# Kernel optimization log

Hardware: AMD Instinct MI355X
Metric: run time of the kernel (lower is better)

Reference implementation:

```python
import jax, jax.numpy as jnp
import numpy as np

B, N, D = 4, 1024, 1024
H, DK, DV = 8, 128, 128
EPS = 1e-6


def setup_inputs() -> dict:
    key = jax.random.key(0)
    ks = jax.random.split(key, 16)
    s = 0.02
    return {
        "q_time": jax.random.normal(ks[0], (B, N, D), jnp.float32),
        "k_time": jax.random.normal(ks[1], (B, N, D), jnp.float32),
        "q_feature": jax.random.normal(ks[2], (B, N, D), jnp.float32),
        "k_feature": jax.random.normal(ks[3], (B, N, D), jnp.float32),
        "v": jax.random.normal(ks[4], (B, N, D), jnp.float32),
        "attn_mask": jax.random.randint(ks[5], (B, N, N), 0, 2, jnp.int32),
        "w_qs_time": jax.random.normal(ks[6], (H * DK, D), jnp.float32) * s,
        "w_ks_time": jax.random.normal(ks[7], (H * DK, D), jnp.float32) * s,
        "w_qs_feature": jax.random.normal(ks[8], (H * DV, D), jnp.float32) * s,
        "w_ks_feature": jax.random.normal(ks[9], (H * DV, D), jnp.float32) * s,
        "w_vs": jax.random.normal(ks[10], (H * DV, D), jnp.float32) * s,
        "w_fc": jax.random.normal(ks[11], (D, H * DV), jnp.float32) * s,
        "ln_gamma": jnp.ones((D,), jnp.float32),
        "ln_beta": jnp.zeros((D,), jnp.float32),
    }


def reference(q_time, k_time, q_feature, k_feature, v, attn_mask,
              w_qs_time, w_ks_time, w_qs_feature, w_ks_feature, w_vs,
              w_fc, ln_gamma, ln_beta):
    temp = DK ** 0.5
    residual = v

    def proj(x, w, d):
        # [B,N,D] @ [D, H*d] -> [B,H,N,d]
        return (x @ w.T).reshape(B, N, H, d).transpose(0, 2, 1, 3)

    qt = proj(q_time, w_qs_time, DK)
    kt = proj(k_time, w_ks_time, DK)
    qf = proj(q_feature, w_qs_feature, DV)
    kf = proj(k_feature, w_ks_feature, DV)
    vv = proj(v, w_vs, DV)

    # time attention: [B,H,N,N]
    attn_time = jnp.einsum('bhnd,bhmd->bhnm', qt / temp, kt)
    attn_time = jnp.where(attn_mask[:, None, :, :] == 0, -1e9, attn_time)
    attn_time = jax.nn.softmax(attn_time, axis=-1)

    # feature attention: q_feature^T @ k_feature -> [B,H,DV,DV]
    attn_feature = jnp.einsum('bhnd,bhne->bhde', qf / temp, kf)
    attn_feature = jax.nn.softmax(attn_feature, axis=-1)

    # chained matmuls: (attn_time @ v) @ attn_feature -> [B,H,N,DV]
    out = jnp.einsum('bhnm,bhmd->bhnd', attn_time, vv)
    out = jnp.einsum('bhnd,bhde->bhne', out, attn_feature)

    out = out.transpose(0, 2, 1, 3).reshape(B, N, H * DV)
    out = out @ w_fc.T + residual  # dropout = identity (eval)

    mean = jnp.mean(out, axis=-1, keepdims=True)
    var = jnp.var(out, axis=-1, keepdims=True)
    out = (out - mean) / jnp.sqrt(var + EPS) * ln_gamma + ln_beta
    return out, attn_time, attn_feature
```

## Files before the change

kernel.cpp:

```cpp
#include <hip/hip_runtime.h>
#include <hip/hip_bf16.h>
#include <cstdint>
#include <cstddef>

typedef unsigned short u16;
typedef unsigned int u32;
typedef short v8s __attribute__((ext_vector_type(8)));
typedef float v4f __attribute__((ext_vector_type(4)));
typedef __hip_bfloat16 bf16;

#define PROJ_ELEMS  4194304ull
#define AT_ELEMS    33554432ull
#define INV_TEMP    0.08838834764831845f

#define GLOBAL_AS __attribute__((address_space(1)))
#define LDS_AS    __attribute__((address_space(3)))

__device__ __forceinline__ void store_out(float* p, float v) { *p = v; }
__device__ __forceinline__ void store_out(bf16* p, float v) { *p = __float2bfloat16(v); }

__device__ __forceinline__ v8s load8f(const float* p) {
    const float4 a = *(const float4*)p;
    const float4 b = *(const float4*)(p + 4);
    v8s r;
    bf16 t;
    t = __float2bfloat16(a.x); r[0] = *(const short*)&t;
    t = __float2bfloat16(a.y); r[1] = *(const short*)&t;
    t = __float2bfloat16(a.z); r[2] = *(const short*)&t;
    t = __float2bfloat16(a.w); r[3] = *(const short*)&t;
    t = __float2bfloat16(b.x); r[4] = *(const short*)&t;
    t = __float2bfloat16(b.y); r[5] = *(const short*)&t;
    t = __float2bfloat16(b.z); r[6] = *(const short*)&t;
    t = __float2bfloat16(b.w); r[7] = *(const short*)&t;
    return r;
}

template <typename AT, typename OutT>
__device__ __forceinline__ void gemm_core(
    const AT* __restrict__ Ab, const u16* __restrict__ Bb, OutT* __restrict__ Cb,
    int K, int lda, int ldb, int ldc, float alpha, int m0, int n0)
{
    __shared__ __align__(16) u16 sA[128][32];
    __shared__ __align__(16) u16 sB[128][32];

    const int tid  = threadIdx.x;
    const int lane = tid & 63;
    const int wid  = tid >> 6;
    const int wm = (wid >> 1) * 64;
    const int wn = (wid & 1) * 64;
    const int quad = lane >> 4;
    const int l16  = lane & 15;

    v4f acc[4][4];
    #pragma unroll
    for (int i = 0; i < 4; ++i)
        #pragma unroll
        for (int j = 0; j < 4; ++j)
            acc[i][j] = (v4f){0.f, 0.f, 0.f, 0.f};

    for (int k0 = 0; k0 < K; k0 += 32) {
        #pragma unroll
        for (int it = 0; it < 2; ++it) {
            const int slot = tid + it * 256;
            const int row  = slot >> 2;
            const int cg   = (slot & 3) << 3;
            __builtin_amdgcn_global_load_lds(
                (const GLOBAL_AS void*)(Bb + (size_t)(n0 + row) * (size_t)ldb + (size_t)(k0 + cg)),
                (LDS_AS void*)((char*)&sB[0][0] + slot * 16), 16, 0, 0);
            if constexpr (sizeof(AT) == 2) {
                __builtin_amdgcn_global_load_lds(
                    (const GLOBAL_AS void*)((const u16*)Ab + (size_t)(m0 + row) * (size_t)lda + (size_t)(k0 + cg)),
                    (LDS_AS void*)((char*)&sA[0][0] + slot * 16), 16, 0, 0);
            } else {
                *(v8s*)&sA[row][cg] =
                    load8f((const float*)Ab + (size_t)(m0 + row) * (size_t)lda + (size_t)(k0 + cg));
            }
        }
        __syncthreads();

        v8s af[4], bfr[4];
        #pragma unroll
        for (int i = 0; i < 4; ++i) {
            af[i]  = *(const v8s*)&sA[wm + i * 16 + l16][quad * 8];
            bfr[i] = *(const v8s*)&sB[wn + i * 16 + l16][quad * 8];
        }
        #pragma unroll
        for (int i = 0; i < 4; ++i)
            #pragma unroll
            for (int j = 0; j < 4; ++j)
                acc[i][j] = __builtin_amdgcn_mfma_f32_16x16x32_bf16(af[i], bfr[j], acc[i][j], 0, 0, 0);
        __syncthreads();
    }

    #pragma unroll
    for (int i = 0; i < 4; ++i) {
        int rbase = m0 + wm + i * 16 + quad * 4;
        #pragma unroll
        for (int j = 0; j < 4; ++j) {
            int gcol = n0 + wn + j * 16 + l16;
            #pragma unroll
            for (int r = 0; r < 4; ++r)
                store_out(&Cb[(size_t)(rbase + r) * (size_t)ldc + (size_t)gcol],
                          acc[i][j][r] * alpha);
        }
    }
}

template <typename AT, typename OutT>
__global__ __launch_bounds__(256, 2)
void gemm_fast(const AT* __restrict__ A, const u16* __restrict__ B, OutT* __restrict__ C,
               int K, int lda, int ldb, int ldc, int batDiv,
               long long sAo, long long sAi, long long sBo, long long sBi,
               long long sCo, long long sCi, float alpha)
{
    const int z  = blockIdx.z;
    const int zo = z / batDiv;
    const int zi = z - zo * batDiv;
    gemm_core<AT, OutT>(A + (size_t)zo * (size_t)sAo + (size_t)zi * (size_t)sAi,
                        B + (size_t)zo * (size_t)sBo + (size_t)zi * (size_t)sBi,
                        C + (size_t)zo * (size_t)sCo + (size_t)zi * (size_t)sCi,
                        K, lda, ldb, ldc, alpha, blockIdx.y * 128, blockIdx.x * 128);
}

struct P5 { const u16* a[5]; };
__global__ __launch_bounds__(256, 2)
void gemm_proj5(P5 As, const u16* __restrict__ W, u16* __restrict__ C)
{
    const int z = blockIdx.z;
    gemm_core<u16, bf16>(As.a[z], W + (size_t)z * 1048576ull,
                         (bf16*)(C + (size_t)z * PROJ_ELEMS),
                         1024, 1024, 1024, 1024, 1.f, blockIdx.y * 128, blockIdx.x * 128);
}

__global__ __launch_bounds__(256, 2)
void gemm_feat_sk(const u16* __restrict__ qfT, const u16* __restrict__ kfT, float* __restrict__ Fp)
{
    const int kc = blockIdx.x, z = blockIdx.y;
    gemm_core<u16, float>(qfT + (size_t)z * 131072ull + (size_t)kc * 128ull,
                          kfT + (size_t)z * 131072ull + (size_t)kc * 128ull,
                          Fp + ((size_t)kc * 32 + z) * 16384ull,
                          128, 1024, 1024, 128, INV_TEMP, 0, 0);
}

template <int NT> struct CP { const float* p[NT]; };

template <int NT>
__global__ __launch_bounds__(256)
void cvt_batch(CP<NT> ps, u16* __restrict__ dst, int perElems)
{
    const float* s = ps.p[blockIdx.z];
    u16* d = dst + (size_t)blockIdx.z * (size_t)perElems;
    const int i = (blockIdx.x * 256 + threadIdx.x) * 8;
    *(v8s*)(d + i) = load8f(s + i);
}

__global__ __launch_bounds__(256)
void mask_pack(const int* __restrict__ mask, u32* __restrict__ mb)
{
    const int w = blockIdx.x * 256 + threadIdx.x;
    const int* src = mask + (size_t)w * 32ull;
    u32 bits = 0;
    #pragma unroll
    for (int i = 0; i < 32; i += 4) {
        int4 v = *(const int4*)(src + i);
        bits |= (u32)(v.x != 0) << i;
        bits |= (u32)(v.y != 0) << (i + 1);
        bits |= (u32)(v.z != 0) << (i + 2);
        bits |= (u32)(v.w != 0) << (i + 3);
    }
    mb[w] = bits;
}

struct T3 { const u16* in[3]; u16* out[3]; };
__global__ __launch_bounds__(256)
void transpose3(T3 t3)
{
    __shared__ u16 tile[32][33];
    const int sel = blockIdx.z >> 5;
    const int z   = blockIdx.z & 31;
    const int b = z >> 3, h = z & 7;
    const u16* ib = t3.in[sel] + (size_t)b * 1048576ull + (size_t)h * 128ull;
    u16* ob = t3.out[sel] + (size_t)z * 131072ull;
    const int m0 = blockIdx.x * 32;
    const int d0 = blockIdx.y * 32;
    const int tx = threadIdx.x;
    const int ty = threadIdx.y;
    #pragma unroll
    for (int i = 0; i < 4; ++i)
        tile[ty + i * 8][tx] = ib[(size_t)(m0 + ty + i * 8) * 1024ull + (size_t)(d0 + tx)];
    __syncthreads();
    #pragma unroll
    for (int i = 0; i < 4; ++i)
        ob[(size_t)(d0 + ty + i * 8) * 1024ull + (size_t)(m0 + tx)] = tile[tx][ty + i * 8];
}

__global__ __launch_bounds__(256, 1)
void fused_attn(const u16* __restrict__ qt, const u16* __restrict__ kt,
                const u16* __restrict__ vvT, const u32* __restrict__ mb,
                float* __restrict__ oAT, u16* __restrict__ opv)
{
    __shared__ __align__(16) u16 sQ[4][128][32];
    __shared__ __align__(16) u16 sT[2][4][128][32];
    __shared__ __align__(16) u16 sP[4][128][40];
    __shared__ u32 smw[2][128][4];

    const int z = blockIdx.y;
    const int b = z >> 3, h = z & 7;
    const int m0 = blockIdx.x * 128;
    const u16* qb = qt + (size_t)b * 1048576ull + (size_t)h * 128ull;
    const u16* kb = kt + (size_t)b * 1048576ull + (size_t)h * 128ull;
    const u16* vb = vvT + (size_t)z * 131072ull;
    float* Ob = oAT + (size_t)z * 1048576ull;
    const u32* mbb = mb + (size_t)b * 32768ull;

    const int tid = threadIdx.x;
    const int lane = tid & 63, wid = tid >> 6;
    const int quad = lane >> 4, l16 = lane & 15;
    const int wm = wid * 32;

    auto stK = [&](int nt, int buf) {
        #pragma unroll
        for (int it = 0; it < 8; ++it) {
            const int slot = tid + it * 256;
            const int ks = slot >> 9, row = (slot >> 2) & 127, cg = (slot & 3) << 3;
            __builtin_amdgcn_global_load_lds(
                (const GLOBAL_AS void*)(kb + (size_t)(nt * 128 + row) * 1024ull + ks * 32 + cg),
                (LDS_AS void*)((char*)&sT[buf][0][0][0] + slot * 16), 16, 0, 0);
        }
    };
    auto stV = [&](int nt, int buf) {
        #pragma unroll
        for (int it = 0; it < 8; ++it) {
            const int slot = tid + it * 256;
            const int ks = slot >> 9, row = (slot >> 2) & 127, cg = (slot & 3) << 3;
            __builtin_amdgcn_global_load_lds(
                (const GLOBAL_AS void*)(vb + (size_t)row * 1024ull + nt * 128 + ks * 32 + cg),
                (LDS_AS void*)((char*)&sT[buf][0][0][0] + slot * 16), 16, 0, 0);
        }
    };
    auto stM = [&](int nt, int buf) {
        #pragma unroll
        for (int it = 0; it < 2; ++it) {
            const int W = wid * 128 + it * 64 + lane;
            __builtin_amdgcn_global_load_lds(
                (const GLOBAL_AS void*)(mbb + (size_t)(m0 + (W >> 2)) * 32ull + nt * 4 + (W & 3)),
                (LDS_AS void*)((char*)&smw[buf][0][0] + W * 4), 4, 0, 0);
        }
    };

    #pragma unroll
    for (int it = 0; it < 8; ++it) {
        const int slot = tid + it * 256;
        const int ks = slot >> 9, row = (slot >> 2) & 127, cg = (slot & 3) << 3;
        __builtin_amdgcn_global_load_lds(
            (const GLOBAL_AS void*)(qb + (size_t)(m0 + row) * 1024ull + ks * 32 + cg),
            (LDS_AS void*)((char*)&sQ[0][0][0] + slot * 16), 16, 0, 0);
    }
    stK(0, 0); stM(0, 0);

    float Mreg[8], Lreg[8];
    #pragma unroll
    for (int x = 0; x < 8; ++x) { Mreg[x] = -3.0e38f; Lreg[x] = 0.f; }

    int bufA = 0, mcur = 0;
    for (int nt = 0; nt < 8; ++nt) {
        stK((nt + 1) & 7, bufA ^ 1);
        stM((nt + 1) & 7, mcur ^ 1);
        asm volatile("s_waitcnt vmcnt(10)" ::: "memory");
        __builtin_amdgcn_s_barrier();
        __builtin_amdgcn_sched_barrier(0);

        v4f acc[2][8];
        #pragma unroll
        for (int i = 0; i < 2; ++i)
            #pragma unroll
            for (int j = 0; j < 8; ++j)
                acc[i][j] = (v4f){0.f, 0.f, 0.f, 0.f};
        #pragma unroll
        for (int ks = 0; ks < 4; ++ks) {
            v8s aq[2], bk[8];
            #pragma unroll
            for (int i = 0; i < 2; ++i)
                aq[i] = *(const v8s*)&sQ[ks][wm + i * 16 + l16][quad * 8];
            #pragma unroll
            for (int j = 0; j < 8; ++j)
                bk[j] = *(const v8s*)&sT[bufA][ks][j * 16 + l16][quad * 8];
            #pragma unroll
            for (int i = 0; i < 2; ++i)
                #pragma unroll
                for (int j = 0; j < 8; ++j)
                    acc[i][j] = __builtin_amdgcn_mfma_f32_16x16x32_bf16(aq[i], bk[j], acc[i][j], 0, 0, 0);
        }

        #pragma unroll
        for (int i = 0; i < 2; ++i)
            #pragma unroll
            for (int r = 0; r < 4; ++r) {
                const int idx = i * 4 + r;
                const int rowl = wm + i * 16 + quad * 4 + r;
                const u32 mw0 = smw[mcur][rowl][0];
                const u32 mw1 = smw[mcur][rowl][1];
                const u32 mw2 = smw[mcur][rowl][2];
                const u32 mw3 = smw[mcur][rowl][3];
                float sv[8];
                float tmax = -3.0e38f;
                #pragma unroll
                for (int j = 0; j < 8; ++j) {
                    const u32 word = (j < 2) ? mw0 : (j < 4) ? mw1 : (j < 6) ? mw2 : mw3;
                    const int bit = ((j & 1) << 4) + l16;
                    float s = acc[i][j][r] * INV_TEMP;
                    s = ((word >> bit) & 1u) ? s : -1e9f;
                    sv[j] = s;
                    tmax = fmaxf(tmax, s);
                }
                #pragma unroll
                for (int m = 1; m <= 8; m <<= 1)
                    tmax = fmaxf(tmax, __shfl_xor(tmax, m));
                const float Mo = Mreg[idx];
                const float Mn = fmaxf(Mo, tmax);
                float t = 0.f;
                #pragma unroll
                for (int j = 0; j < 8; ++j)
                    t += __expf(sv[j] - Mn);
                #pragma unroll
                for (int m = 1; m <= 8; m <<= 1)
                    t += __shfl_xor(t, m);
                Lreg[idx] = Lreg[idx] * __expf(Mo - Mn) + t;
                Mreg[idx] = Mn;
            }

        asm volatile("s_waitcnt lgkmcnt(0)" ::: "memory");
        __builtin_amdgcn_s_barrier();
        __builtin_amdgcn_sched_barrier(0);
        bufA ^= 1; mcur ^= 1;
    }

    float IL[8];
    #pragma unroll
    for (int x = 0; x < 8; ++x) IL[x] = 1.f / Lreg[x];

    const int BK = bufA;
    const int BV = BK ^ 1;

    v4f pacc[2][8];
    #pragma unroll
    for (int i = 0; i < 2; ++i)
        #pragma unroll
        for (int j = 0; j < 8; ++j)
            pacc[i][j] = (v4f){0.f, 0.f, 0.f, 0.f};

    for (int nt = 0; nt < 8; ++nt) {
        stV(nt, BV);
        asm volatile("s_waitcnt vmcnt(8)" ::: "memory");
        __builtin_amdgcn_s_barrier();
        __builtin_amdgcn_sched_barrier(0);

        v4f acc[2][8];
        #pragma unroll
        for (int i = 0; i < 2; ++i)
            #pragma unroll
            for (int j = 0; j < 8; ++j)
                acc[i][j] = (v4f){0.f, 0.f, 0.f, 0.f};
        #pragma unroll
        for (int ks = 0; ks < 4; ++ks) {
            v8s aq[2], bk[8];
            #pragma unroll
            for (int i = 0; i < 2; ++i)
                aq[i] = *(const v8s*)&sQ[ks][wm + i * 16 + l16][quad * 8];
            #pragma unroll
            for (int j = 0; j < 8; ++j)
                bk[j] = *(const v8s*)&sT[BK][ks][j * 16 + l16][quad * 8];
            #pragma unroll
            for (int i = 0; i < 2; ++i)
                #pragma unroll
                for (int j = 0; j < 8; ++j)
                    acc[i][j] = __builtin_amdgcn_mfma_f32_16x16x32_bf16(aq[i], bk[j], acc[i][j], 0, 0, 0);
        }

        asm volatile("s_waitcnt lgkmcnt(0)" ::: "memory");
        __builtin_amdgcn_s_barrier();
        __builtin_amdgcn_sched_barrier(0);

        if (nt < 7) {
            stK(nt + 1, BK);
            stM(nt + 1, mcur ^ 1);
            asm volatile("s_waitcnt vmcnt(10)" ::: "memory");
        } else {
            asm volatile("s_waitcnt vmcnt(0)" ::: "memory");
        }

        #pragma unroll
        for (int i = 0; i < 2; ++i)
            #pragma unroll
            for (int r = 0; r < 4; ++r) {
                const int idx = i * 4 + r;
                const int rowl = wm + i * 16 + quad * 4 + r;
                const u32 mw0 = smw[mcur][rowl][0];
                const u32 mw1 = smw[mcur][rowl][1];
                const u32 mw2 = smw[mcur][rowl][2];
                const u32 mw3 = smw[mcur][rowl][3];
                float* orow = Ob + (size_t)(m0 + rowl) * 1024ull + nt * 128;
                #pragma unroll
                for (int j = 0; j < 8; ++j) {
                    const u32 word = (j < 2) ? mw0 : (j < 4) ? mw1 : (j < 6) ? mw2 : mw3;
                    const int bit = ((j & 1) << 4) + l16;
                    float s = acc[i][j][r] * INV_TEMP;
                    s = ((word >> bit) & 1u) ? s : -1e9f;
                    const float p = __expf(s - Mreg[idx]) * IL[idx];
                    orow[j * 16 + l16] = p;
                    bf16 pb = __float2bfloat16(p);
                    sP[j >> 1][rowl][((j & 1) << 4) + l16] = *(const u16*)&pb;
                }
            }

        asm volatile("s_waitcnt lgkmcnt(0)" ::: "memory");
        __builtin_amdgcn_s_barrier();
        __builtin_amdgcn_sched_barrier(0);

        #pragma unroll
        for (int ks = 0; ks < 4; ++ks) {
            v8s ap[2], bv[8];
            #pragma unroll
            for (int i = 0; i < 2; ++i)
                ap[i] = *(const v8s*)&sP[ks][wm + i * 16 + l16][quad * 8];
            #pragma unroll
            for (int j = 0; j < 8; ++j)
                bv[j] = *(const v8s*)&sT[BV][ks][j * 16 + l16][quad * 8];
            #pragma unroll
            for (int i = 0; i < 2; ++i)
                #pragma unroll
                for (int j = 0; j < 8; ++j)
                    pacc[i][j] = __builtin_amdgcn_mfma_f32_16x16x32_bf16(ap[i], bv[j], pacc[i][j], 0, 0, 0);
        }

        asm volatile("s_waitcnt lgkmcnt(0)" ::: "memory");
        __builtin_amdgcn_s_barrier();
        __builtin_amdgcn_sched_barrier(0);
        mcur ^= 1;
    }

    u16* opvB = opv + (size_t)z * 131072ull;
    #pragma unroll
    for (int i = 0; i < 2; ++i) {
        const int rbase = m0 + wm + i * 16 + quad * 4;
        #pragma unroll
        for (int j = 0; j < 8; ++j) {
            const int e = j * 16 + l16;
            #pragma unroll
            for (int r = 0; r < 4; ++r) {
                bf16 t = __float2bfloat16(pacc[i][j][r]);
                opvB[(size_t)(rbase + r) * 128ull + e] = *(const u16*)&t;
            }
        }
    }
}

__global__ __launch_bounds__(128)
void softmax_feat(const float* __restrict__ Fp, float* __restrict__ out_af, u16* __restrict__ FT)
{
    const int r = blockIdx.x;
    const int z = r >> 7, d = r & 127;
    const int e = threadIdx.x;
    float x = 0.f;
    #pragma unroll
    for (int kc = 0; kc < 8; ++kc)
        x += Fp[((size_t)kc * 32 + z) * 16384ull + (size_t)d * 128ull + e];
    float mx = x;
    #pragma unroll
    for (int o = 32; o; o >>= 1) mx = fmaxf(mx, __shfl_xor(mx, o));
    __shared__ float redm[2], reds[2];
    const int w = e >> 6;
    if ((e & 63) == 0) redm[w] = mx;
    __syncthreads();
    mx = fmaxf(redm[0], redm[1]);
    float ex = __expf(x - mx);
    float s = ex;
    #pragma unroll
    for (int o = 32; o; o >>= 1) s += __shfl_xor(s, o);
    if ((e & 63) == 0) reds[w] = s;
    __syncthreads();
    s = reds[0] + reds[1];
    float p = ex / s;
    out_af[(size_t)r * 128ull + e] = p;
    bf16 pb = __float2bfloat16(p);
    FT[(size_t)z * 16384ull + (size_t)e * 128ull + d] = *(const u16*)&pb;
}

__global__ __launch_bounds__(256)
void resid_ln(const float* __restrict__ fc, const float* __restrict__ v,
              const float* __restrict__ gamma, const float* __restrict__ beta,
              float* __restrict__ out)
{
    const int r = blockIdx.x;
    const int t = threadIdx.x;
    const float4* fr = (const float4*)(fc + (size_t)r * 1024ull);
    const float4* vr = (const float4*)(v  + (size_t)r * 1024ull);
    float4 a = fr[t], b4 = vr[t];
    float4 x = {a.x + b4.x, a.y + b4.y, a.z + b4.z, a.w + b4.w};
    float s  = x.x + x.y + x.z + x.w;
    float s2 = x.x * x.x + x.y * x.y + x.z * x.z + x.w * x.w;
    #pragma unroll
    for (int o = 32; o; o >>= 1) { s += __shfl_xor(s, o); s2 += __shfl_xor(s2, o); }
    __shared__ float rs[4], rs2[4];
    const int w = t >> 6;
    if ((t & 63) == 0) { rs[w] = s; rs2[w] = s2; }
    __syncthreads();
    s  = rs[0] + rs[1] + rs[2] + rs[3];
    s2 = rs2[0] + rs2[1] + rs2[2] + rs2[3];
    const float mean = s * (1.f / 1024.f);
    const float var  = s2 * (1.f / 1024.f) - mean * mean;
    const float rstd = rsqrtf(var + 1e-6f);
    const float4 g = ((const float4*)gamma)[t];
    const float4 bb = ((const float4*)beta)[t];
    float4 o4 = {(x.x - mean) * rstd * g.x + bb.x,
                 (x.y - mean) * rstd * g.y + bb.y,
                 (x.z - mean) * rstd * g.z + bb.z,
                 (x.w - mean) * rstd * g.w + bb.w};
    ((float4*)(out + (size_t)r * 1024ull))[t] = o4;
}

extern "C" void kernel_launch(void* const* d_in, const int* in_sizes, int n_in,
                              void* d_out, int out_size, void* d_ws, size_t ws_size,
                              hipStream_t stream)
{
    (void)in_sizes; (void)n_in; (void)out_size; (void)ws_size;
    const float* q_time    = (const float*)d_in[0];
    const float* k_time    = (const float*)d_in[1];
    const float* q_feature = (const float*)d_in[2];
    const float* k_feature = (const float*)d_in[3];
    const float* v_in      = (const float*)d_in[4];
    const int*   mask      = (const int*)d_in[5];
    const float* w_qs_t    = (const float*)d_in[6];
    const float* w_ks_t    = (const float*)d_in[7];
    const float* w_qs_f    = (const float*)d_in[8];
    const float* w_ks_f    = (const float*)d_in[9];
    const float* w_vs      = (const float*)d_in[10];
    const float* w_fc      = (const float*)d_in[11];
    const float* gamma     = (const float*)d_in[12];
    const float* beta      = (const float*)d_in[13];

    char* ws = (char*)d_ws;
    const size_t MB = 1ull << 20;
    u16*   act = (u16*)(ws + 0  * MB);
    u16*   wbf = (u16*)(ws + 40 * MB);
    u16*   qt  = (u16*)(ws + 52 * MB);
    u16*   vvT = (u16*)(ws + 0  * MB);
    u16*   qfT = (u16*)(ws + 8  * MB);
    u16*   kfT = (u16*)(ws + 16 * MB);
    u16*   FT  = (u16*)(ws + 24 * MB);
    float* Fp  = (float*)(ws + 25 * MB);
    u16*   opv = (u16*)(ws + 41 * MB);
    u16*   o2  = (u16*)(ws + 52 * MB);
    float* fc  = (float*)(ws + 60 * MB);
    u32*   mb  = (u32*)(ws + 92 * MB);
    u16*   kt  = qt + PROJ_ELEMS;
    u16*   qf  = kt + PROJ_ELEMS;
    u16*   kf  = qf + PROJ_ELEMS;
    u16*   vv  = kf + PROJ_ELEMS;
    u16*   wfc = wbf + 5ull * 1048576ull;

    float* out0 = (float*)d_out;
    float* oAT  = out0 + PROJ_ELEMS;
    float* oAF  = out0 + PROJ_ELEMS + AT_ELEMS;

    const dim3 blk(256);

    {
        CP<5> ca; ca.p[0] = q_time; ca.p[1] = k_time; ca.p[2] = q_feature;
                  ca.p[3] = k_feature; ca.p[4] = v_in;
        cvt_batch<5><<<dim3(2048, 1, 5), blk, 0, stream>>>(ca, act, 4194304);
        CP<6> cw; cw.p[0] = w_qs_t; cw.p[1] = w_ks_t; cw.p[2] = w_qs_f;
                  cw.p[3] = w_ks_f; cw.p[4] = w_vs; cw.p[5] = w_fc;
        cvt_batch<6><<<dim3(512, 1, 6), blk, 0, stream>>>(cw, wbf, 1048576);
        mask_pack<<<512, blk, 0, stream>>>(mask, mb);
    }

    {
        P5 ps; for (int i = 0; i < 5; ++i) ps.a[i] = act + (size_t)i * PROJ_ELEMS;
        gemm_proj5<<<dim3(8, 32, 5), blk, 0, stream>>>(ps, wbf, qt);
    }

    {
        T3 t3; t3.in[0] = vv; t3.in[1] = qf; t3.in[2] = kf;
               t3.out[0] = vvT; t3.out[1] = qfT; t3.out[2] = kfT;
        transpose3<<<dim3(32, 4, 96), dim3(32, 8, 1), 0, stream>>>(t3);
    }

    gemm_feat_sk<<<dim3(8, 32), blk, 0, stream>>>(qfT, kfT, Fp);

    softmax_feat<<<4096, 128, 0, stream>>>(Fp, oAF, FT);

    fused_attn<<<dim3(8, 32), blk, 0, stream>>>(qt, kt, vvT, mb, oAT, opv);

    gemm_fast<<<dim3(1, 8, 32), blk, 0, stream>>>(opv, FT, (bf16*)o2, 128,
        128, 128, 1024, 8, 1048576LL, 131072LL, 131072LL, 16384LL, 1048576LL, 128LL, 1.f);

    gemm_fast<<<dim3(8, 32, 1), blk, 0, stream>>>(o2, wfc, fc, 1024, 1024, 1024, 1024, 1,
        0LL, 0LL, 0LL, 0LL, 0LL, 0LL, 1.f);

    resid_ln<<<4096, 256, 0, stream>>>(fc, v_in, gamma, beta, out0);
}
```

Before: 466.7 us.

## Use 512-thread attention blocks and XCD-aware block remapping across GEMMs

The fused attention kernel moves from 4 waves per block, each owning 32 query rows, to 8 waves per block, each owning 16 rows. This halves per-wave accumulators and loads and lets more waves overlap memory latency. The projection, final fc GEMM and attention kernels also remap flat block IDs so that blocks sharing operands land on the same XCD, to improve L2 reuse. The trade-off is more barrier participants and smaller per-wave MFMA tiles, which lowers operand reuse from LDS.

```diff
diff --git a/kernel.cpp b/kernel.cpp
--- a/kernel.cpp
+++ b/kernel.cpp
@@ -111,25 +111,39 @@
 void gemm_fast(const AT* __restrict__ A, const u16* __restrict__ B, OutT* __restrict__ C,
                int K, int lda, int ldb, int ldc, int batDiv,
                long long sAo, long long sAi, long long sBo, long long sBi,
-               long long sCo, long long sCi, float alpha)
+               long long sCo, long long sCi, float alpha, int swz)
 {
     const int z  = blockIdx.z;
     const int zo = z / batDiv;
     const int zi = z - zo * batDiv;
+    int bx, by;
+    if (swz) {
+        const int flat = blockIdx.x + (blockIdx.y << 3);
+        const int xcd = flat & 7, slt = flat >> 3;
+        by = xcd + ((slt >> 3) << 3);
+        bx = slt & 7;
+    } else {
+        bx = blockIdx.x; by = blockIdx.y;
+    }
     gemm_core<AT, OutT>(A + (size_t)zo * (size_t)sAo + (size_t)zi * (size_t)sAi,
                         B + (size_t)zo * (size_t)sBo + (size_t)zi * (size_t)sBi,
                         C + (size_t)zo * (size_t)sCo + (size_t)zi * (size_t)sCi,
-                        K, lda, ldb, ldc, alpha, blockIdx.y * 128, blockIdx.x * 128);
+                        K, lda, ldb, ldc, alpha, by * 128, bx * 128);
 }
 
 struct P5 { const u16* a[5]; };
 __global__ __launch_bounds__(256, 2)
 void gemm_proj5(P5 As, const u16* __restrict__ W, u16* __restrict__ C)
 {
-    const int z = blockIdx.z;
+    const int fid = blockIdx.x + (blockIdx.y << 3) + (blockIdx.z << 8);
+    const int xcd = fid & 7, s = fid >> 3;
+    const int p = ((s >> 3) << 3) + xcd;
+    const int bx = s & 7;
+    const int by = p & 31;
+    const int z  = p >> 5;
     gemm_core<u16, bf16>(As.a[z], W + (size_t)z * 1048576ull,
                          (bf16*)(C + (size_t)z * PROJ_ELEMS),
-                         1024, 1024, 1024, 1024, 1.f, blockIdx.y * 128, blockIdx.x * 128);
+                         1024, 1024, 1024, 1024, 1.f, by * 128, bx * 128);
 }
 
 __global__ __launch_bounds__(256, 2)
@@ -194,7 +208,7 @@
         ob[(size_t)(d0 + ty + i * 8) * 1024ull + (size_t)(m0 + tx)] = tile[tx][ty + i * 8];
 }
 
-__global__ __launch_bounds__(256, 1)
+__global__ __launch_bounds__(512, 2)
 void fused_attn(const u16* __restrict__ qt, const u16* __restrict__ kt,
                 const u16* __restrict__ vvT, const u32* __restrict__ mb,
                 float* __restrict__ oAT, u16* __restrict__ opv)
@@ -204,9 +218,12 @@
     __shared__ __align__(16) u16 sP[4][128][40];
     __shared__ u32 smw[2][128][4];
 
-    const int z = blockIdx.y;
+    const int flat = blockIdx.x + (blockIdx.y << 3);
+    const int xcd = flat & 7, slt = flat >> 3;
+    const int z  = xcd + ((slt >> 3) << 3);
+    const int m0 = (slt & 7) << 7;
+
     const int b = z >> 3, h = z & 7;
-    const int m0 = blockIdx.x * 128;
     const u16* qb = qt + (size_t)b * 1048576ull + (size_t)h * 128ull;
     const u16* kb = kt + (size_t)b * 1048576ull + (size_t)h * 128ull;
     const u16* vb = vvT + (size_t)z * 131072ull;
@@ -216,118 +233,106 @@
     const int tid = threadIdx.x;
     const int lane = tid & 63, wid = tid >> 6;
     const int quad = lane >> 4, l16 = lane & 15;
-    const int wm = wid * 32;
+    const int wm = wid << 4;
 
     auto stK = [&](int nt, int buf) {
         #pragma unroll
-        for (int it = 0; it < 8; ++it) {
-            const int slot = tid + it * 256;
-            const int ks = slot >> 9, row = (slot >> 2) & 127, cg = (slot & 3) << 3;
+        for (int it = 0; it < 4; ++it) {
+            const int s2 = tid + it * 512;
+            const int ks = s2 >> 9, row = (s2 >> 2) & 127, cg = (s2 & 3) << 3;
             __builtin_amdgcn_global_load_lds(
                 (const GLOBAL_AS void*)(kb + (size_t)(nt * 128 + row) * 1024ull + ks * 32 + cg),
-                (LDS_AS void*)((char*)&sT[buf][0][0][0] + slot * 16), 16, 0, 0);
+                (LDS_AS void*)((char*)&sT[buf][0][0][0] + s2 * 16), 16, 0, 0);
         }
     };
     auto stV = [&](int nt, int buf) {
         #pragma unroll
-        for (int it = 0; it < 8; ++it) {
-            const int slot = tid + it * 256;
-            const int ks = slot >> 9, row = (slot >> 2) & 127, cg = (slot & 3) << 3;
+        for (int it = 0; it < 4; ++it) {
+            const int s2 = tid + it * 512;
+            const int ks = s2 >> 9, row = (s2 >> 2) & 127, cg = (s2 & 3) << 3;
             __builtin_amdgcn_global_load_lds(
                 (const GLOBAL_AS void*)(vb + (size_t)row * 1024ull + nt * 128 + ks * 32 + cg),
-                (LDS_AS void*)((char*)&sT[buf][0][0][0] + slot * 16), 16, 0, 0);
+                (LDS_AS void*)((char*)&sT[buf][0][0][0] + s2 * 16), 16, 0, 0);
         }
     };
     auto stM = [&](int nt, int buf) {
-        #pragma unroll
-        for (int it = 0; it < 2; ++it) {
-            const int W = wid * 128 + it * 64 + lane;
-            __builtin_amdgcn_global_load_lds(
-                (const GLOBAL_AS void*)(mbb + (size_t)(m0 + (W >> 2)) * 32ull + nt * 4 + (W & 3)),
-                (LDS_AS void*)((char*)&smw[buf][0][0] + W * 4), 4, 0, 0);
-        }
+        const int W = tid;
+        __builtin_amdgcn_global_load_lds(
+            (const GLOBAL_AS void*)(mbb + (size_t)(m0 + (W >> 2)) * 32ull + nt * 4 + (W & 3)),
+            (LDS_AS void*)((char*)&smw[buf][0][0] + W * 4), 4, 0, 0);
     };
 
     #pragma unroll
-    for (int it = 0; it < 8; ++it) {
-        const int slot = tid + it * 256;
-        const int ks = slot >> 9, row = (slot >> 2) & 127, cg = (slot & 3) << 3;
+    for (int it = 0; it < 4; ++it) {
+        const int s2 = tid + it * 512;
+        const int ks = s2 >> 9, row = (s2 >> 2) & 127, cg = (s2 & 3) << 3;
         __builtin_amdgcn_global_load_lds(
             (const GLOBAL_AS void*)(qb + (size_t)(m0 + row) * 1024ull + ks * 32 + cg),
-            (LDS_AS void*)((char*)&sQ[0][0][0] + slot * 16), 16, 0, 0);
+            (LDS_AS void*)((char*)&sQ[0][0][0] + s2 * 16), 16, 0, 0);
     }
     stK(0, 0); stM(0, 0);
 
-    float Mreg[8], Lreg[8];
-    #pragma unroll
-    for (int x = 0; x < 8; ++x) { Mreg[x] = -3.0e38f; Lreg[x] = 0.f; }
+    float Mreg[4], Lreg[4];
+    #pragma unroll
+    for (int x = 0; x < 4; ++x) { Mreg[x] = -3.0e38f; Lreg[x] = 0.f; }
 
     int bufA = 0, mcur = 0;
     for (int nt = 0; nt < 8; ++nt) {
         stK((nt + 1) & 7, bufA ^ 1);
         stM((nt + 1) & 7, mcur ^ 1);
-        asm volatile("s_waitcnt vmcnt(10)" ::: "memory");
+        asm volatile("s_waitcnt vmcnt(5)" ::: "memory");
         __builtin_amdgcn_s_barrier();
         __builtin_amdgcn_sched_barrier(0);
 
-        v4f acc[2][8];
-        #pragma unroll
-        for (int i = 0; i < 2; ++i)
-            #pragma unroll
-            for (int j = 0; j < 8; ++j)
-                acc[i][j] = (v4f){0.f, 0.f, 0.f, 0.f};
+        v4f acc[8];
+        #pragma unroll
+        for (int j = 0; j < 8; ++j)
+            acc[j] = (v4f){0.f, 0.f, 0.f, 0.f};
         #pragma unroll
         for (int ks = 0; ks < 4; ++ks) {
-            v8s aq[2], bk[8];
-            #pragma unroll
-            for (int i = 0; i < 2; ++i)
-                aq[i] = *(const v8s*)&sQ[ks][wm + i * 16 + l16][quad * 8];
+            const v8s aq = *(const v8s*)&sQ[ks][wm + l16][quad * 8];
+            v8s bk[8];
             #pragma unroll
             for (int j = 0; j < 8; ++j)
                 bk[j] = *(const v8s*)&sT[bufA][ks][j * 16 + l16][quad * 8];
             #pragma unroll
-            for (int i = 0; i < 2; ++i)
-                #pragma unroll
-                for (int j = 0; j < 8; ++j)
-                    acc[i][j] = __builtin_amdgcn_mfma_f32_16x16x32_bf16(aq[i], bk[j], acc[i][j], 0, 0, 0);
-        }
-
-        #pragma unroll
-        for (int i = 0; i < 2; ++i)
-            #pragma unroll
-            for (int r = 0; r < 4; ++r) {
-                const int idx = i * 4 + r;
-                const int rowl = wm + i * 16 + quad * 4 + r;
-                const u32 mw0 = smw[mcur][rowl][0];
-                const u32 mw1 = smw[mcur][rowl][1];
-                const u32 mw2 = smw[mcur][rowl][2];
-                const u32 mw3 = smw[mcur][rowl][3];
-                float sv[8];
-                float tmax = -3.0e38f;
-                #pragma unroll
-                for (int j = 0; j < 8; ++j) {
-                    const u32 word = (j < 2) ? mw0 : (j < 4) ? mw1 : (j < 6) ? mw2 : mw3;
-                    const int bit = ((j & 1) << 4) + l16;
-                    float s = acc[i][j][r] * INV_TEMP;
-                    s = ((word >> bit) & 1u) ? s : -1e9f;
-                    sv[j] = s;
-                    tmax = fmaxf(tmax, s);
-                }
-                #pragma unroll
-                for (int m = 1; m <= 8; m <<= 1)
-                    tmax = fmaxf(tmax, __shfl_xor(tmax, m));
-                const float Mo = Mreg[idx];
-                const float Mn = fmaxf(Mo, tmax);
-                float t = 0.f;
-                #pragma unroll
-                for (int j = 0; j < 8; ++j)
-                    t += __expf(sv[j] - Mn);
-                #pragma unroll
-                for (int m = 1; m <= 8; m <<= 1)
-                    t += __shfl_xor(t, m);
-                Lreg[idx] = Lreg[idx] * __expf(Mo - Mn) + t;
-                Mreg[idx] = Mn;
+            for (int j = 0; j < 8; ++j)
+                acc[j] = __builtin_amdgcn_mfma_f32_16x16x32_bf16(aq, bk[j], acc[j], 0, 0, 0);
+        }
+
+        #pragma unroll
+        for (int r = 0; r < 4; ++r) {
+            const int rowl = wm + quad * 4 + r;
+            const u32 mw0 = smw[mcur][rowl][0];
+            const u32 mw1 = smw[mcur][rowl][1];
+            const u32 mw2 = smw[mcur][rowl][2];
+            const u32 mw3 = smw[mcur][rowl][3];
+            float sv[8];
+            float tmax = -3.0e38f;
+            #pragma unroll
+            for (int j = 0; j < 8; ++j) {
+                const u32 word = (j < 2) ? mw0 : (j < 4) ? mw1 : (j < 6) ? mw2 : mw3;
+                const int bit = ((j & 1) << 4) + l16;
+                float s = acc[j][r] * INV_TEMP;
+                s = ((word >> bit) & 1u) ? s : -1e9f;
+                sv[j] = s;
+                tmax = fmaxf(tmax, s);
             }
+            #pragma unroll
+            for (int m = 1; m <= 8; m <<= 1)
+                tmax = fmaxf(tmax, __shfl_xor(tmax, m));
+            const float Mo = Mreg[r];
+            const float Mn = fmaxf(Mo, tmax);
+            float t = 0.f;
+            #pragma unroll
+            for (int j = 0; j < 8; ++j)
+                t += __expf(sv[j] - Mn);
+            #pragma unroll
+            for (int m = 1; m <= 8; m <<= 1)
+                t += __shfl_xor(t, m);
+            Lreg[r] = Lreg[r] * __expf(Mo - Mn) + t;
+            Mreg[r] = Mn;
+        }
 
         asm volatile("s_waitcnt lgkmcnt(0)" ::: "memory");
         __builtin_amdgcn_s_barrier();
@@ -335,46 +340,38 @@
         bufA ^= 1; mcur ^= 1;
     }
 
-    float IL[8];
-    #pragma unroll
-    for (int x = 0; x < 8; ++x) IL[x] = 1.f / Lreg[x];
+    float IL[4];
+    #pragma unroll
+    for (int x = 0; x < 4; ++x) IL[x] = 1.f / Lreg[x];
 
     const int BK = bufA;
     const int BV = BK ^ 1;
 
-    v4f pacc[2][8];
-    #pragma unroll
-    for (int i = 0; i < 2; ++i)
-        #pragma unroll
-        for (int j = 0; j < 8; ++j)
-            pacc[i][j] = (v4f){0.f, 0.f, 0.f, 0.f};
+    v4f pacc[8];
+    #pragma unroll
+    for (int j = 0; j < 8; ++j)
+        pacc[j] = (v4f){0.f, 0.f, 0.f, 0.f};
 
     for (int nt = 0; nt < 8; ++nt) {
         stV(nt, BV);
-        asm volatile("s_waitcnt vmcnt(8)" ::: "memory");
+        asm volatile("s_waitcnt vmcnt(4)" ::: "memory");
         __builtin_amdgcn_s_barrier();
         __builtin_amdgcn_sched_barrier(0);
 
-        v4f acc[2][8];
-        #pragma unroll
-        for (int i = 0; i < 2; ++i)
-            #pragma unroll
-            for (int j = 0; j < 8; ++j)
-                acc[i][j] = (v4f){0.f, 0.f, 0.f, 0.f};
+        v4f acc[8];
+        #pragma unroll
+        for (int j = 0; j < 8; ++j)
+            acc[j] = (v4f){0.f, 0.f, 0.f, 0.f};
         #pragma unroll
         for (int ks = 0; ks < 4; ++ks) {
-            v8s aq[2], bk[8];
-            #pragma unroll
-            for (int i = 0; i < 2; ++i)
-                aq[i] = *(const v8s*)&sQ[ks][wm + i * 16 + l16][quad * 8];
+            const v8s aq = *(const v8s*)&sQ[ks][wm + l16][quad * 8];
+            v8s bk[8];
             #pragma unroll
             for (int j = 0; j < 8; ++j)
                 bk[j] = *(const v8s*)&sT[BK][ks][j * 16 + l16][quad * 8];
             #pragma unroll
-            for (int i = 0; i < 2; ++i)
-                #pragma unroll
-                for (int j = 0; j < 8; ++j)
-                    acc[i][j] = __builtin_amdgcn_mfma_f32_16x16x32_bf16(aq[i], bk[j], acc[i][j], 0, 0, 0);
+            for (int j = 0; j < 8; ++j)
+                acc[j] = __builtin_amdgcn_mfma_f32_16x16x32_bf16(aq, bk[j], acc[j], 0, 0, 0);
         }
 
         asm volatile("s_waitcnt lgkmcnt(0)" ::: "memory");
@@ -384,34 +381,31 @@
         if (nt < 7) {
             stK(nt + 1, BK);
             stM(nt + 1, mcur ^ 1);
-            asm volatile("s_waitcnt vmcnt(10)" ::: "memory");
+            asm volatile("s_waitcnt vmcnt(5)" ::: "memory");
         } else {
             asm volatile("s_waitcnt vmcnt(0)" ::: "memory");
         }
 
         #pragma unroll
-        for (int i = 0; i < 2; ++i)
-            #pragma unroll
-            for (int r = 0; r < 4; ++r) {
-                const int idx = i * 4 + r;
-                const int rowl = wm + i * 16 + quad * 4 + r;
-                const u32 mw0 = smw[mcur][rowl][0];
-                const u32 mw1 = smw[mcur][rowl][1];
-                const u32 mw2 = smw[mcur][rowl][2];
-                const u32 mw3 = smw[mcur][rowl][3];
-                float* orow = Ob + (size_t)(m0 + rowl) * 1024ull + nt * 128;
-                #pragma unroll
-                for (int j = 0; j < 8; ++j) {
-                    const u32 word = (j < 2) ? mw0 : (j < 4) ? mw1 : (j < 6) ? mw2 : mw3;
-                    const int bit = ((j & 1) << 4) + l16;
-                    float s = acc[i][j][r] * INV_TEMP;
-                    s = ((word >> bit) & 1u) ? s : -1e9f;
-                    const float p = __expf(s - Mreg[idx]) * IL[idx];
-                    orow[j * 16 + l16] = p;
-                    bf16 pb = __float2bfloat16(p);
-                    sP[j >> 1][rowl][((j & 1) << 4) + l16] = *(const u16*)&pb;
-                }
+        for (int r = 0; r < 4; ++r) {
+            const int rowl = wm + quad * 4 + r;
+            const u32 mw0 = smw[mcur][rowl][0];
+            const u32 mw1 = smw[mcur][rowl][1];
+            const u32 mw2 = smw[mcur][rowl][2];
+            const u32 mw3 = smw[mcur][rowl][3];
+            float* orow = Ob + (size_t)(m0 + rowl) * 1024ull + nt * 128;
+            #pragma unroll
+            for (int j = 0; j < 8; ++j) {
+                const u32 word = (j < 2) ? mw0 : (j < 4) ? mw1 : (j < 6) ? mw2 : mw3;
+                const int bit = ((j & 1) << 4) + l16;
+                float s = acc[j][r] * INV_TEMP;
+                s = ((word >> bit) & 1u) ? s : -1e9f;
+                const float p = __expf(s - Mreg[r]) * IL[r];
+                orow[j * 16 + l16] = p;
+                bf16 pb = __float2bfloat16(p);
+                sP[j >> 1][rowl][((j & 1) << 4) + l16] = *(const u16*)&pb;
             }
+        }
 
         asm volatile("s_waitcnt lgkmcnt(0)" ::: "memory");
         __builtin_amdgcn_s_barrier();
@@ -419,18 +413,14 @@
 
         #pragma unroll
         for (int ks = 0; ks < 4; ++ks) {
-            v8s ap[2], bv[8];
-            #pragma unroll
-            for (int i = 0; i < 2; ++i)
-                ap[i] = *(const v8s*)&sP[ks][wm + i * 16 + l16][quad * 8];
+            const v8s ap = *(const v8s*)&sP[ks][wm + l16][quad * 8];
+            v8s bv[8];
             #pragma unroll
             for (int j = 0; j < 8; ++j)
                 bv[j] = *(const v8s*)&sT[BV][ks][j * 16 + l16][quad * 8];
             #pragma unroll
-            for (int i = 0; i < 2; ++i)
-                #pragma unroll
-                for (int j = 0; j < 8; ++j)
-                    pacc[i][j] = __builtin_amdgcn_mfma_f32_16x16x32_bf16(ap[i], bv[j], pacc[i][j], 0, 0, 0);
+            for (int j = 0; j < 8; ++j)
+                pacc[j] = __builtin_amdgcn_mfma_f32_16x16x32_bf16(ap, bv[j], pacc[j], 0, 0, 0);
         }
 
         asm volatile("s_waitcnt lgkmcnt(0)" ::: "memory");
@@ -440,17 +430,14 @@
     }
 
     u16* opvB = opv + (size_t)z * 131072ull;
-    #pragma unroll
-    for (int i = 0; i < 2; ++i) {
-        const int rbase = m0 + wm + i * 16 + quad * 4;
-        #pragma unroll
-        for (int j = 0; j < 8; ++j) {
-            const int e = j * 16 + l16;
-            #pragma unroll
-            for (int r = 0; r < 4; ++r) {
-                bf16 t = __float2bfloat16(pacc[i][j][r]);
-                opvB[(size_t)(rbase + r) * 128ull + e] = *(const u16*)&t;
-            }
+    const int rbase = m0 + wm + quad * 4;
+    #pragma unroll
+    for (int j = 0; j < 8; ++j) {
+        const int e = j * 16 + l16;
+        #pragma unroll
+        for (int r = 0; r < 4; ++r) {
+            bf16 t = __float2bfloat16(pacc[j][r]);
+            opvB[(size_t)(rbase + r) * 128ull + e] = *(const u16*)&t;
         }
     }
 }
@@ -590,13 +577,13 @@
 
     softmax_feat<<<4096, 128, 0, stream>>>(Fp, oAF, FT);
 
-    fused_attn<<<dim3(8, 32), blk, 0, stream>>>(qt, kt, vvT, mb, oAT, opv);
+    fused_attn<<<dim3(8, 32), dim3(512), 0, stream>>>(qt, kt, vvT, mb, oAT, opv);
 
     gemm_fast<<<dim3(1, 8, 32), blk, 0, stream>>>(opv, FT, (bf16*)o2, 128,
-        128, 128, 1024, 8, 1048576LL, 131072LL, 131072LL, 16384LL, 1048576LL, 128LL, 1.f);
+        128, 128, 1024, 8, 1048576LL, 131072LL, 131072LL, 16384LL, 1048576LL, 128LL, 1.f, 0);
 
     gemm_fast<<<dim3(8, 32, 1), blk, 0, stream>>>(o2, wfc, fc, 1024, 1024, 1024, 1024, 1,
-        0LL, 0LL, 0LL, 0LL, 0LL, 0LL, 1.f);
+        0LL, 0LL, 0LL, 0LL, 0LL, 0LL, 1.f, 1);
 
     resid_ln<<<4096, 256, 0, stream>>>(fc, v_in, gamma, beta, out0);
 }
```

After: 441.7 us. 1.06x faster.
